# Kernel optimization log

Measured on AMD Instinct MI355X. Metric: run time of the kernel, lower is better.

## Reference

```python
import math
import jax, jax.numpy as jnp
import numpy as np

H = 16
D_MODEL = 1024
D_K = D_MODEL // H


def setup_inputs() -> dict:
    key = jax.random.key(0)
    ks = jax.random.split(key, 12)
    B, S = 4, 2048
    scale = 1.0 / math.sqrt(D_MODEL)
    inp = {
        "query": jax.random.normal(ks[0], (B, S, D_MODEL), jnp.float32),
        "key": jax.random.normal(ks[1], (B, S, D_MODEL), jnp.float32),
        "value": jax.random.normal(ks[2], (B, S, D_MODEL), jnp.float32),
        "mask": jnp.ones((B, 1, 1, S), jnp.int32),
        "Wq": jax.random.normal(ks[3], (D_MODEL, D_MODEL), jnp.float32) * scale,
        "bq": jnp.zeros((D_MODEL,), jnp.float32),
        "Wk": jax.random.normal(ks[4], (D_MODEL, D_MODEL), jnp.float32) * scale,
        "bk": jnp.zeros((D_MODEL,), jnp.float32),
        "Wv": jax.random.normal(ks[5], (D_MODEL, D_MODEL), jnp.float32) * scale,
        "bv": jnp.zeros((D_MODEL,), jnp.float32),
        "Wo": jax.random.normal(ks[6], (D_MODEL, D_MODEL), jnp.float32) * scale,
        "bo": jnp.zeros((D_MODEL,), jnp.float32),
    }
    return inp


def _split_heads(x, W, b):
    # x: (B, S, d_model) -> (B, H, S, d_k); torch Linear: x @ W.T + b
    B, S, _ = x.shape
    y = x @ W.T + b
    return y.reshape(B, S, H, D_K).transpose(0, 2, 1, 3)


def reference(query, key, value, mask, Wq, bq, Wk, bk, Wv, bv, Wo, bo):
    B, Sq, _ = query.shape
    q = _split_heads(query, Wq, bq)   # (B,H,Sq,dk)
    k = _split_heads(key, Wk, bk)     # (B,H,Skv,dk)
    v = _split_heads(value, Wv, bv)   # (B,H,Skv,dk)
    scores = jnp.einsum('bhqd,bhkd->bhqk', q, k) / math.sqrt(D_K)
    scores = jnp.where(mask == 0, jnp.float32(-1e9), scores)
    p_attn = jax.nn.softmax(scores, axis=-1)  # dropout p=0 (eval)
    x = jnp.einsum('bhqk,bhkd->bhqd', p_attn, v)
    x = x.transpose(0, 2, 1, 3).reshape(B, Sq, H * D_K)
    return x @ Wo.T + bo
```

## Files before the change

### kernel.cpp

```cpp
#include <hip/hip_runtime.h>
#include <hip/hip_bf16.h>
#include <stdint.h>

typedef unsigned short u16;
typedef short bf16x8 __attribute__((ext_vector_type(8)));
typedef float f32x4 __attribute__((ext_vector_type(4)));

#define D_MODEL 1024
#define NHEAD 16
#define DK 64
#define SEQ 2048
#define NB 4
#define MTOT (NB * SEQ)

__device__ __forceinline__ u16 f2bf(float f) {
  union { float f; unsigned u; } x; x.f = f;
  unsigned r = x.u + 0x7FFFu + ((x.u >> 16) & 1u);
  return (u16)(r >> 16);
}
#if __has_builtin(__builtin_amdgcn_cvt_pk_bf16_f32)
__device__ __forceinline__ unsigned pkbf(float a, float b) {
  auto r = __builtin_amdgcn_cvt_pk_bf16_f32(a, b);
  union { decltype(r) v; unsigned u; } c; c.v = r; return c.u;
}
#else
__device__ __forceinline__ unsigned pkbf(float a, float b) {
  return (unsigned)f2bf(a) | ((unsigned)f2bf(b) << 16);
}
#endif
#if __has_builtin(__builtin_amdgcn_exp2f)
__device__ __forceinline__ float exp2r(float x) { return __builtin_amdgcn_exp2f(x); }
#else
__device__ __forceinline__ float exp2r(float x) { return exp2f(x); }
#endif
__device__ __forceinline__ void gl_lds16(const u16* g, u16* s) {
  __builtin_amdgcn_global_load_lds(
      (const __attribute__((address_space(1))) void*)g,
      (__attribute__((address_space(3))) void*)s, 16, 0, 0);
}

struct CvtArgs {
  const float4* s[7];
  uint2* d[7];
  int n4[7];
};
__global__ __launch_bounds__(256) void cvt_all(CvtArgs a) {
  const int y = blockIdx.y;
  const float4* s = a.s[y];
  uint2* d = a.d[y];
  const int n4 = a.n4[y];
  for (int i = blockIdx.x * 256 + threadIdx.x; i < n4; i += gridDim.x * 256) {
    float4 x = s[i];
    uint2 o;
    o.x = pkbf(x.x, x.y);
    o.y = pkbf(x.z, x.w);
    d[i] = o;
  }
}
__global__ __launch_bounds__(256) void cvt1(const float4* __restrict__ src,
                                            uint2* __restrict__ dst, int n4) {
  for (int i = blockIdx.x * 256 + threadIdx.x; i < n4; i += gridDim.x * 256) {
    float4 x = src[i];
    uint2 o;
    o.x = pkbf(x.x, x.y);
    o.y = pkbf(x.z, x.w);
    dst[i] = o;
  }
}
__global__ __launch_bounds__(256) void cvt4(const float4* __restrict__ s0,
                                            const float4* __restrict__ s1,
                                            const float4* __restrict__ s2,
                                            const float4* __restrict__ s3,
                                            uint2* __restrict__ dst, int n4each) {
  const float4* s = (blockIdx.y == 0) ? s0 : (blockIdx.y == 1) ? s1
                  : (blockIdx.y == 2) ? s2 : s3;
  uint2* d = dst + (size_t)blockIdx.y * n4each;
  for (int i = blockIdx.x * 256 + threadIdx.x; i < n4each; i += gridDim.x * 256) {
    float4 x = s[i];
    uint2 o;
    o.x = pkbf(x.x, x.y);
    o.y = pkbf(x.z, x.w);
    d[i] = o;
  }
}

template <int MODE>
__device__ __forceinline__ void gemm_body(
    const u16* __restrict__ A, const u16* __restrict__ W,
    const float* __restrict__ bias, void* __restrict__ out, float scale,
    int m0, int n0, u16* smem)
{
  u16* As = smem;
  u16* Bs = smem + 4096;

  const int tid = threadIdx.x;
  const int l = tid & 63, w = tid >> 6;
  const int lq = l & 15, qd = l >> 4;
  const int wm = (w >> 1) << 5, wn = (w & 1) << 6;

  int arow[2], ak8[2], brow[4], bk8[4];
#pragma unroll
  for (int r = 0; r < 2; ++r) {
    int c = r * 256 + tid;
    arow[r] = c >> 3; ak8[r] = (c & 7) ^ (arow[r] & 7);
  }
#pragma unroll
  for (int r = 0; r < 4; ++r) {
    int c = r * 256 + tid;
    brow[r] = c >> 3; bk8[r] = (c & 7) ^ (brow[r] & 7);
  }
  int aoff[2][2], boff[4][2];
#pragma unroll
  for (int i = 0; i < 2; ++i) {
    int mr = wm + (i << 4) + lq;
#pragma unroll
    for (int s = 0; s < 2; ++s)
      aoff[i][s] = (mr << 6) + ((((s << 2) + qd) ^ (mr & 7)) << 3);
  }
#pragma unroll
  for (int j = 0; j < 4; ++j) {
    int nr = wn + (j << 4) + lq;
#pragma unroll
    for (int s = 0; s < 2; ++s)
      boff[j][s] = (nr << 6) + ((((s << 2) + qd) ^ (nr & 7)) << 3);
  }

  const u16* Ab = A + (size_t)m0 * D_MODEL;
  const u16* Bb = W + (size_t)n0 * D_MODEL;

  f32x4 acc[2][4] = {};

  for (int kt = 0; kt < 16; ++kt) {
    const int kbase = kt << 6;
#pragma unroll
    for (int r = 0; r < 2; ++r)
      gl_lds16(Ab + (size_t)arow[r] * D_MODEL + kbase + (ak8[r] << 3), As + ((r * 256 + tid) << 3));
#pragma unroll
    for (int r = 0; r < 4; ++r)
      gl_lds16(Bb + (size_t)brow[r] * D_MODEL + kbase + (bk8[r] << 3), Bs + ((r * 256 + tid) << 3));
    __syncthreads();
#pragma unroll
    for (int s = 0; s < 2; ++s) {
      bf16x8 af[2], bfv[4];
#pragma unroll
      for (int i = 0; i < 2; ++i) af[i] = *(const bf16x8*)(As + aoff[i][s]);
#pragma unroll
      for (int j = 0; j < 4; ++j) bfv[j] = *(const bf16x8*)(Bs + boff[j][s]);
#pragma unroll
      for (int i = 0; i < 2; ++i)
#pragma unroll
        for (int j = 0; j < 4; ++j)
          acc[i][j] = __builtin_amdgcn_mfma_f32_16x16x32_bf16(af[i], bfv[j], acc[i][j], 0, 0, 0);
    }
    __syncthreads();
  }

  if (MODE == 1) {
    u16* Cs = smem;
    u16* outb = (u16*)out;
#pragma unroll
    for (int i = 0; i < 2; ++i)
#pragma unroll
      for (int j = 0; j < 4; ++j) {
        int ml = wm + (i << 4) + (qd << 2);
        int nl = wn + (j << 4) + lq;
        float bj = bias[n0 + nl];
        uint2 pk;
        pk.x = pkbf(acc[i][j][0] + bj, acc[i][j][1] + bj);
        pk.y = pkbf(acc[i][j][2] + bj, acc[i][j][3] + bj);
        *(uint2*)(Cs + nl * 80 + ml) = pk;
      }
    __syncthreads();
    int nl = tid >> 1, sh = (tid & 1) << 5;
    int n = n0 + nl;
    int b_ = m0 >> 11;
    const uint4* src = (const uint4*)(Cs + nl * 80 + sh);
    uint4* dst = (uint4*)(outb +
        (((size_t)b_ * NHEAD + (n >> 6)) * DK + (n & 63)) * SEQ + (m0 & 2047) + sh);
#pragma unroll
    for (int e = 0; e < 4; ++e) dst[e] = src[e];
  } else {
    u16* outb = (u16*)out;
    float* outf = (float*)out;
#pragma unroll
    for (int i = 0; i < 2; ++i)
#pragma unroll
      for (int j = 0; j < 4; ++j) {
        int ml = m0 + wm + (i << 4) + (qd << 2);
        int n = n0 + wn + (j << 4) + lq;
        float bj = bias[n];
#pragma unroll
        for (int r = 0; r < 4; ++r) {
          int m = ml + r;
          float v = (acc[i][j][r] + bj) * scale;
          if (MODE == 0)
            outb[(((size_t)(m >> 11) * NHEAD + (n >> 6)) * SEQ + (m & 2047)) * DK + (n & 63)] = f2bf(v);
          else
            outf[(size_t)m * D_MODEL + n] = v;
        }
      }
  }
}

template <int MODE>
__global__ __launch_bounds__(256, 4) void gemm_bt64(
    const u16* __restrict__ A, const u16* __restrict__ W,
    const float* __restrict__ bias, void* __restrict__ out, float scale)
{
  __shared__ alignas(16) u16 smem[12288];
  gemm_body<MODE>(A, W, bias, out, scale,
                  blockIdx.y << 6, blockIdx.x << 7, smem);
}

__global__ __launch_bounds__(256, 4) void proj_qkv(
    const u16* __restrict__ Cq, const u16* __restrict__ Ck, const u16* __restrict__ Cv,
    const u16* __restrict__ wq, const u16* __restrict__ wk, const u16* __restrict__ wv,
    const float* __restrict__ bq, const float* __restrict__ bk, const float* __restrict__ bv,
    u16* __restrict__ Qb, u16* __restrict__ Kb, u16* __restrict__ Vt, float scq)
{
  __shared__ alignas(16) u16 smem[12288];
  const int z = blockIdx.z;
  const int m0 = blockIdx.y << 6, n0 = blockIdx.x << 7;
  if (z == 0)
    gemm_body<0>(Cq, wq, bq, Qb, scq, m0, n0, smem);
  else if (z == 1)
    gemm_body<0>(Ck, wk, bk, Kb, 1.0f, m0, n0, smem);
  else
    gemm_body<1>(Cv, wv, bv, Vt, 1.0f, m0, n0, smem);
}

__global__ __launch_bounds__(256, 4) void attn_fused(
    const u16* __restrict__ Q,
    const u16* __restrict__ K,
    const u16* __restrict__ Vt,
    const int* __restrict__ mask,
    u16* __restrict__ X)
{
  __shared__ alignas(16) u16 PQ[8192];
  __shared__ alignas(16) u16 Ks[4096];
  __shared__ alignas(16) u16 Vs[5120];
  __shared__ alignas(16) float mbf[64];

  const int tid = threadIdx.x;
  const int l = tid & 63, w = tid >> 6;
  const int lq = l & 15, qd = l >> 4;
  const int bh = blockIdx.y;
  const int q0 = blockIdx.x << 7;
  const int b_ = bh >> 4, h = bh & 15;
  const size_t base = (size_t)bh * SEQ * DK;
  const int wq0 = w << 5;

#pragma unroll
  for (int r = 0; r < 4; ++r) {
    int c = r * 256 + tid;
    int row = c >> 3, k8 = (c & 7) ^ (row & 7);
    gl_lds16(Q + base + (size_t)(q0 + row) * DK + (k8 << 3), PQ + (c << 3));
  }
  {
    unsigned v = (tid < 16) ? 0x3F803F80u : 0u;
    uint2 pk; pk.x = v; pk.y = v;
    *(uint2*)(Vs + 4096 + tid * 4) = pk;
  }
  __syncthreads();

  bf16x8 qf[2][2];
#pragma unroll
  for (int i = 0; i < 2; ++i)
#pragma unroll
    for (int s = 0; s < 2; ++s) {
      int row = wq0 + (i << 4) + lq;
      qf[i][s] = *(const bf16x8*)(PQ + (row << 6) + ((((s << 2) + qd) ^ (row & 7)) << 3));
    }

  f32x4 Ov[2][4] = {};
  f32x4 Ovl[2] = {};

  for (int t = 0; t < 32; ++t) {
    const int kv0 = t << 6;
    __syncthreads();
#pragma unroll
    for (int r = 0; r < 2; ++r) {
      int c = r * 256 + tid;
      int row = c >> 3, k8 = (c & 7) ^ (row & 7);
      gl_lds16(K + base + (size_t)(kv0 + row) * DK + (k8 << 3), Ks + (c << 3));
    }
#pragma unroll
    for (int r = 0; r < 2; ++r) {
      int c = r * 256 + tid;
      int row = c >> 3, k8 = (c & 7) ^ (row & 7);
      gl_lds16(Vt + base + (size_t)row * SEQ + kv0 + (k8 << 3), Vs + (c << 3));
    }
    if (tid < 64)
      mbf[tid] = mask[b_ * SEQ + kv0 + tid] ? 0.0f : -1.44269504e9f;
    __syncthreads();

    float4 m4[4];
#pragma unroll
    for (int jb = 0; jb < 4; ++jb) m4[jb] = *(const float4*)(mbf + (jb << 4) + (qd << 2));

    f32x4 Sc[4][2];
#pragma unroll
    for (int jb = 0; jb < 4; ++jb)
#pragma unroll
      for (int i = 0; i < 2; ++i) {
        Sc[jb][i][0] = m4[jb].x; Sc[jb][i][1] = m4[jb].y;
        Sc[jb][i][2] = m4[jb].z; Sc[jb][i][3] = m4[jb].w;
      }
#pragma unroll
    for (int s = 0; s < 2; ++s) {
      bf16x8 kf[4];
#pragma unroll
      for (int jb = 0; jb < 4; ++jb) {
        int row = (jb << 4) + lq;
        kf[jb] = *(const bf16x8*)(Ks + (row << 6) + ((((s << 2) + qd) ^ (row & 7)) << 3));
      }
#pragma unroll
      for (int jb = 0; jb < 4; ++jb)
#pragma unroll
        for (int i = 0; i < 2; ++i)
          Sc[jb][i] = __builtin_amdgcn_mfma_f32_16x16x32_bf16(kf[jb], qf[i][s], Sc[jb][i], 0, 0, 0);
    }

#pragma unroll
    for (int i = 0; i < 2; ++i) {
      const int prow = wq0 + (i << 4) + lq;
      const int rbase = prow << 6;
      const int rsw = prow & 7;
#pragma unroll
      for (int jb = 0; jb < 4; ++jb) {
        float p0 = exp2r(Sc[jb][i][0]);
        float p1 = exp2r(Sc[jb][i][1]);
        float p2 = exp2r(Sc[jb][i][2]);
        float p3 = exp2r(Sc[jb][i][3]);
        uint2 pk;
        pk.x = pkbf(p0, p1);
        pk.y = pkbf(p2, p3);
        int c = (jb << 1) + (qd >> 1);
        *(uint2*)(PQ + rbase + ((c ^ rsw) << 3) + ((qd & 1) << 2)) = pk;
      }
    }

#pragma unroll
    for (int s = 0; s < 2; ++s) {
      bf16x8 pf[2], vf[4], vf1;
#pragma unroll
      for (int i = 0; i < 2; ++i) {
        int prow = wq0 + (i << 4) + lq;
        pf[i] = *(const bf16x8*)(PQ + (prow << 6) + ((((s << 2) + qd) ^ (prow & 7)) << 3));
      }
#pragma unroll
      for (int j = 0; j < 4; ++j) {
        int row = (j << 4) + lq;
        vf[j] = *(const bf16x8*)(Vs + (row << 6) + ((((s << 2) + qd) ^ (row & 7)) << 3));
      }
      {
        int row = 64 + lq;
        vf1 = *(const bf16x8*)(Vs + (row << 6) + ((((s << 2) + qd) ^ (row & 7)) << 3));
      }
#pragma unroll
      for (int i = 0; i < 2; ++i) {
#pragma unroll
        for (int j = 0; j < 4; ++j)
          Ov[i][j] = __builtin_amdgcn_mfma_f32_16x16x32_bf16(pf[i], vf[j], Ov[i][j], 0, 0, 0);
        Ovl[i] = __builtin_amdgcn_mfma_f32_16x16x32_bf16(pf[i], vf1, Ovl[i], 0, 0, 0);
      }
    }
  }

#pragma unroll
  for (int i = 0; i < 2; ++i) {
    float inv[4];
#pragma unroll
    for (int r = 0; r < 4; ++r) inv[r] = 1.0f / Ovl[i][r];
#pragma unroll
    for (int r = 0; r < 4; ++r) {
      float sc_ = __shfl(inv[r], l & 48);
      int qrow = q0 + wq0 + (i << 4) + (qd << 2) + r;
#pragma unroll
      for (int j = 0; j < 4; ++j)
        X[((size_t)b_ * SEQ + qrow) * D_MODEL + (h << 6) + (j << 4) + lq] =
            f2bf(Ov[i][j][r] * sc_);
    }
  }
}

extern "C" void kernel_launch(void* const* d_in, const int* in_sizes, int n_in,
                              void* d_out, int out_size, void* d_ws, size_t ws_size,
                              hipStream_t stream) {
  const float* query = (const float*)d_in[0];
  const float* key_  = (const float*)d_in[1];
  const float* value = (const float*)d_in[2];
  const int* mask    = (const int*)d_in[3];
  const float* Wq = (const float*)d_in[4];
  const float* bq = (const float*)d_in[5];
  const float* Wk = (const float*)d_in[6];
  const float* bk = (const float*)d_in[7];
  const float* Wv = (const float*)d_in[8];
  const float* bv = (const float*)d_in[9];
  const float* Wo = (const float*)d_in[10];
  const float* bo = (const float*)d_in[11];

  u16* ws16 = (u16*)d_ws;
  const size_t WSZ = (size_t)D_MODEL * D_MODEL;
  const size_t ASZ = (size_t)MTOT * D_MODEL;
  const float SCQ = 0.125f * 1.44269504088896f;

  dim3 blk(256);
  dim3 gg(D_MODEL / 128, MTOT / 64);

  if (ws_size >= (size_t)(4 * WSZ + 4 * ASZ) * 2) {
    u16* wqc = ws16;
    u16* wkc = ws16 + WSZ;
    u16* wvc = ws16 + 2 * WSZ;
    u16* woc = ws16 + 3 * WSZ;
    u16* Cq  = ws16 + 4 * WSZ;
    u16* Ck  = ws16 + 4 * WSZ + ASZ;
    u16* Qb  = ws16 + 4 * WSZ + 2 * ASZ;
    u16* Kb  = ws16 + 4 * WSZ + 3 * ASZ;
    u16* Xb  = Cq;
    u16* Vtb = (u16*)d_out;
    u16* Cv  = (u16*)d_out + ASZ;

    CvtArgs ca;
    ca.s[0] = (const float4*)query; ca.d[0] = (uint2*)Cq;  ca.n4[0] = (int)(ASZ / 4);
    ca.s[1] = (const float4*)key_;  ca.d[1] = (uint2*)Ck;  ca.n4[1] = (int)(ASZ / 4);
    ca.s[2] = (const float4*)value; ca.d[2] = (uint2*)Cv;  ca.n4[2] = (int)(ASZ / 4);
    ca.s[3] = (const float4*)Wq;    ca.d[3] = (uint2*)wqc; ca.n4[3] = (int)(WSZ / 4);
    ca.s[4] = (const float4*)Wk;    ca.d[4] = (uint2*)wkc; ca.n4[4] = (int)(WSZ / 4);
    ca.s[5] = (const float4*)Wv;    ca.d[5] = (uint2*)wvc; ca.n4[5] = (int)(WSZ / 4);
    ca.s[6] = (const float4*)Wo;    ca.d[6] = (uint2*)woc; ca.n4[6] = (int)(WSZ / 4);

    cvt_all<<<dim3(512, 7), blk, 0, stream>>>(ca);
    proj_qkv<<<dim3(D_MODEL / 128, MTOT / 64, 3), blk, 0, stream>>>(
        Cq, Ck, Cv, wqc, wkc, wvc, bq, bk, bv, Qb, Kb, Vtb, SCQ);
    attn_fused<<<dim3(SEQ / 128, NB * NHEAD), blk, 0, stream>>>(Qb, Kb, Vtb, mask, Xb);
    gemm_bt64<2><<<gg, blk, 0, stream>>>(Xb, woc, bo, d_out, 1.0f);
  } else {
    u16* wqc = ws16;
    u16* wkc = ws16 + WSZ;
    u16* wvc = ws16 + 2 * WSZ;
    u16* woc = ws16 + 3 * WSZ;
    u16* C1  = ws16 + 4 * WSZ;
    u16* Qb  = ws16 + 4 * WSZ + ASZ;
    u16* Kb  = ws16 + 4 * WSZ + 2 * ASZ;
    u16* Xb  = C1;
    u16* Vtb = (u16*)d_out;

    cvt4<<<dim3(256, 4), blk, 0, stream>>>((const float4*)Wq, (const float4*)Wk,
                                           (const float4*)Wv, (const float4*)Wo,
                                           (uint2*)wqc, (int)(WSZ / 4));
    cvt1<<<1024, blk, 0, stream>>>((const float4*)query, (uint2*)C1, (int)(ASZ / 4));
    gemm_bt64<0><<<gg, blk, 0, stream>>>(C1, wqc, bq, Qb, SCQ);
    cvt1<<<1024, blk, 0, stream>>>((const float4*)key_, (uint2*)C1, (int)(ASZ / 4));
    gemm_bt64<0><<<gg, blk, 0, stream>>>(C1, wkc, bk, Kb, 1.0f);
    cvt1<<<1024, blk, 0, stream>>>((const float4*)value, (uint2*)C1, (int)(ASZ / 4));
    gemm_bt64<1><<<gg, blk, 0, stream>>>(C1, wvc, bv, Vtb, 1.0f);
    attn_fused<<<dim3(SEQ / 128, NB * NHEAD), blk, 0, stream>>>(Qb, Kb, Vtb, mask, Xb);
    gemm_bt64<2><<<gg, blk, 0, stream>>>(Xb, woc, bo, d_out, 1.0f);
  }
}
```

Measured before the change: 349.6 us.

## Enlarge GEMM tiles to 128x128 and reorder grids for M-major block scheduling

The shared GEMM body moves from a 64x128 to a 128x128 output tile, with each wave computing a 64x64 sub-tile (4x4 MFMA fragments). The aim is more data reuse per LDS load and fewer global loads per FLOP. Grid dimensions for the projection, output GEMM and attention kernels are swapped, so consecutive blocks walk M (or batch-head) first, which changes cache locality of the shared weight and K/V tiles. The cost is a larger shared-memory footprint and more accumulator registers, and the occupancy hint of 4 blocks per CU is dropped. The fallback path reuses cvt_all in place of the removed cvt1/cvt4 kernels.

```diff
diff --git a/kernel.cpp b/kernel.cpp
--- a/kernel.cpp
+++ b/kernel.cpp
@@ -57,32 +57,6 @@
     d[i] = o;
   }
 }
-__global__ __launch_bounds__(256) void cvt1(const float4* __restrict__ src,
-                                            uint2* __restrict__ dst, int n4) {
-  for (int i = blockIdx.x * 256 + threadIdx.x; i < n4; i += gridDim.x * 256) {
-    float4 x = src[i];
-    uint2 o;
-    o.x = pkbf(x.x, x.y);
-    o.y = pkbf(x.z, x.w);
-    dst[i] = o;
-  }
-}
-__global__ __launch_bounds__(256) void cvt4(const float4* __restrict__ s0,
-                                            const float4* __restrict__ s1,
-                                            const float4* __restrict__ s2,
-                                            const float4* __restrict__ s3,
-                                            uint2* __restrict__ dst, int n4each) {
-  const float4* s = (blockIdx.y == 0) ? s0 : (blockIdx.y == 1) ? s1
-                  : (blockIdx.y == 2) ? s2 : s3;
-  uint2* d = dst + (size_t)blockIdx.y * n4each;
-  for (int i = blockIdx.x * 256 + threadIdx.x; i < n4each; i += gridDim.x * 256) {
-    float4 x = s[i];
-    uint2 o;
-    o.x = pkbf(x.x, x.y);
-    o.y = pkbf(x.z, x.w);
-    d[i] = o;
-  }
-}
 
 template <int MODE>
 __device__ __forceinline__ void gemm_body(
@@ -91,63 +65,56 @@
     int m0, int n0, u16* smem)
 {
   u16* As = smem;
-  u16* Bs = smem + 4096;
+  u16* Bs = smem + 8192;
 
   const int tid = threadIdx.x;
   const int l = tid & 63, w = tid >> 6;
-  const int lq = l & 15, qd = l >> 4;
-  const int wm = (w >> 1) << 5, wn = (w & 1) << 6;
-
-  int arow[2], ak8[2], brow[4], bk8[4];
-#pragma unroll
-  for (int r = 0; r < 2; ++r) {
-    int c = r * 256 + tid;
-    arow[r] = c >> 3; ak8[r] = (c & 7) ^ (arow[r] & 7);
-  }
+  const int wm = (w >> 1) << 6, wn = (w & 1) << 6;
+
+  int srow[4], sk8[4], sdst[4];
 #pragma unroll
   for (int r = 0; r < 4; ++r) {
     int c = r * 256 + tid;
-    brow[r] = c >> 3; bk8[r] = (c & 7) ^ (brow[r] & 7);
-  }
-  int aoff[2][2], boff[4][2];
-#pragma unroll
-  for (int i = 0; i < 2; ++i) {
-    int mr = wm + (i << 4) + lq;
-#pragma unroll
-    for (int s = 0; s < 2; ++s)
-      aoff[i][s] = (mr << 6) + ((((s << 2) + qd) ^ (mr & 7)) << 3);
-  }
-#pragma unroll
-  for (int j = 0; j < 4; ++j) {
-    int nr = wn + (j << 4) + lq;
-#pragma unroll
-    for (int s = 0; s < 2; ++s)
-      boff[j][s] = (nr << 6) + ((((s << 2) + qd) ^ (nr & 7)) << 3);
+    srow[r] = c >> 3;
+    sk8[r] = (c & 7) ^ (srow[r] & 7);
+    sdst[r] = c << 3;
+  }
+  int aoff[4][2], boff[4][2];
+#pragma unroll
+  for (int i = 0; i < 4; ++i) {
+    int mr = wm + (i << 4) + (l & 15);
+    int nr = wn + (i << 4) + (l & 15);
+#pragma unroll
+    for (int s = 0; s < 2; ++s) {
+      int kc = (s << 2) + (l >> 4);
+      aoff[i][s] = (mr << 6) + ((kc ^ (mr & 7)) << 3);
+      boff[i][s] = (nr << 6) + ((kc ^ (nr & 7)) << 3);
+    }
   }
 
   const u16* Ab = A + (size_t)m0 * D_MODEL;
   const u16* Bb = W + (size_t)n0 * D_MODEL;
 
-  f32x4 acc[2][4] = {};
+  f32x4 acc[4][4] = {};
 
   for (int kt = 0; kt < 16; ++kt) {
     const int kbase = kt << 6;
 #pragma unroll
-    for (int r = 0; r < 2; ++r)
-      gl_lds16(Ab + (size_t)arow[r] * D_MODEL + kbase + (ak8[r] << 3), As + ((r * 256 + tid) << 3));
-#pragma unroll
     for (int r = 0; r < 4; ++r)
-      gl_lds16(Bb + (size_t)brow[r] * D_MODEL + kbase + (bk8[r] << 3), Bs + ((r * 256 + tid) << 3));
+      gl_lds16(Ab + (size_t)srow[r] * D_MODEL + kbase + (sk8[r] << 3), As + sdst[r]);
+#pragma unroll
+    for (int r = 0; r < 4; ++r)
+      gl_lds16(Bb + (size_t)srow[r] * D_MODEL + kbase + (sk8[r] << 3), Bs + sdst[r]);
     __syncthreads();
 #pragma unroll
     for (int s = 0; s < 2; ++s) {
-      bf16x8 af[2], bfv[4];
-#pragma unroll
-      for (int i = 0; i < 2; ++i) af[i] = *(const bf16x8*)(As + aoff[i][s]);
+      bf16x8 af[4], bfv[4];
+#pragma unroll
+      for (int i = 0; i < 4; ++i) af[i] = *(const bf16x8*)(As + aoff[i][s]);
 #pragma unroll
       for (int j = 0; j < 4; ++j) bfv[j] = *(const bf16x8*)(Bs + boff[j][s]);
 #pragma unroll
-      for (int i = 0; i < 2; ++i)
+      for (int i = 0; i < 4; ++i)
 #pragma unroll
         for (int j = 0; j < 4; ++j)
           acc[i][j] = __builtin_amdgcn_mfma_f32_16x16x32_bf16(af[i], bfv[j], acc[i][j], 0, 0, 0);
@@ -159,35 +126,35 @@
     u16* Cs = smem;
     u16* outb = (u16*)out;
 #pragma unroll
-    for (int i = 0; i < 2; ++i)
+    for (int i = 0; i < 4; ++i)
 #pragma unroll
       for (int j = 0; j < 4; ++j) {
-        int ml = wm + (i << 4) + (qd << 2);
-        int nl = wn + (j << 4) + lq;
+        int sl = wm + (i << 4) + ((l >> 4) << 2);
+        int nl = wn + (j << 4) + (l & 15);
         float bj = bias[n0 + nl];
         uint2 pk;
         pk.x = pkbf(acc[i][j][0] + bj, acc[i][j][1] + bj);
         pk.y = pkbf(acc[i][j][2] + bj, acc[i][j][3] + bj);
-        *(uint2*)(Cs + nl * 80 + ml) = pk;
+        *(uint2*)(Cs + nl * 136 + sl) = pk;
       }
     __syncthreads();
-    int nl = tid >> 1, sh = (tid & 1) << 5;
+    int nl = tid >> 1, sh = (tid & 1) << 6;
     int n = n0 + nl;
     int b_ = m0 >> 11;
-    const uint4* src = (const uint4*)(Cs + nl * 80 + sh);
+    const uint4* src = (const uint4*)(Cs + nl * 136 + sh);
     uint4* dst = (uint4*)(outb +
         (((size_t)b_ * NHEAD + (n >> 6)) * DK + (n & 63)) * SEQ + (m0 & 2047) + sh);
 #pragma unroll
-    for (int e = 0; e < 4; ++e) dst[e] = src[e];
+    for (int e = 0; e < 8; ++e) dst[e] = src[e];
   } else {
     u16* outb = (u16*)out;
     float* outf = (float*)out;
 #pragma unroll
-    for (int i = 0; i < 2; ++i)
+    for (int i = 0; i < 4; ++i)
 #pragma unroll
       for (int j = 0; j < 4; ++j) {
-        int ml = m0 + wm + (i << 4) + (qd << 2);
-        int n = n0 + wn + (j << 4) + lq;
+        int ml = m0 + wm + (i << 4) + ((l >> 4) << 2);
+        int n = n0 + wn + (j << 4) + (l & 15);
         float bj = bias[n];
 #pragma unroll
         for (int r = 0; r < 4; ++r) {
@@ -203,24 +170,24 @@
 }
 
 template <int MODE>
-__global__ __launch_bounds__(256, 4) void gemm_bt64(
+__global__ __launch_bounds__(256) void gemm128(
     const u16* __restrict__ A, const u16* __restrict__ W,
     const float* __restrict__ bias, void* __restrict__ out, float scale)
 {
-  __shared__ alignas(16) u16 smem[12288];
+  __shared__ alignas(16) u16 smem[17408];
   gemm_body<MODE>(A, W, bias, out, scale,
-                  blockIdx.y << 6, blockIdx.x << 7, smem);
-}
-
-__global__ __launch_bounds__(256, 4) void proj_qkv(
+                  blockIdx.x << 7, blockIdx.y << 7, smem);
+}
+
+__global__ __launch_bounds__(256) void proj_qkv(
     const u16* __restrict__ Cq, const u16* __restrict__ Ck, const u16* __restrict__ Cv,
     const u16* __restrict__ wq, const u16* __restrict__ wk, const u16* __restrict__ wv,
     const float* __restrict__ bq, const float* __restrict__ bk, const float* __restrict__ bv,
     u16* __restrict__ Qb, u16* __restrict__ Kb, u16* __restrict__ Vt, float scq)
 {
-  __shared__ alignas(16) u16 smem[12288];
+  __shared__ alignas(16) u16 smem[17408];
   const int z = blockIdx.z;
-  const int m0 = blockIdx.y << 6, n0 = blockIdx.x << 7;
+  const int m0 = blockIdx.x << 7, n0 = blockIdx.y << 7;
   if (z == 0)
     gemm_body<0>(Cq, wq, bq, Qb, scq, m0, n0, smem);
   else if (z == 1)
@@ -244,8 +211,8 @@
   const int tid = threadIdx.x;
   const int l = tid & 63, w = tid >> 6;
   const int lq = l & 15, qd = l >> 4;
-  const int bh = blockIdx.y;
-  const int q0 = blockIdx.x << 7;
+  const int bh = blockIdx.x;
+  const int q0 = blockIdx.y << 7;
   const int b_ = bh >> 4, h = bh & 15;
   const size_t base = (size_t)bh * SEQ * DK;
   const int wq0 = w << 5;
@@ -406,7 +373,7 @@
   const float SCQ = 0.125f * 1.44269504088896f;
 
   dim3 blk(256);
-  dim3 gg(D_MODEL / 128, MTOT / 64);
+  dim3 gg(MTOT / 128, D_MODEL / 128);
 
   if (ws_size >= (size_t)(4 * WSZ + 4 * ASZ) * 2) {
     u16* wqc = ws16;
@@ -431,10 +398,10 @@
     ca.s[6] = (const float4*)Wo;    ca.d[6] = (uint2*)woc; ca.n4[6] = (int)(WSZ / 4);
 
     cvt_all<<<dim3(512, 7), blk, 0, stream>>>(ca);
-    proj_qkv<<<dim3(D_MODEL / 128, MTOT / 64, 3), blk, 0, stream>>>(
+    proj_qkv<<<dim3(MTOT / 128, D_MODEL / 128, 3), blk, 0, stream>>>(
         Cq, Ck, Cv, wqc, wkc, wvc, bq, bk, bv, Qb, Kb, Vtb, SCQ);
-    attn_fused<<<dim3(SEQ / 128, NB * NHEAD), blk, 0, stream>>>(Qb, Kb, Vtb, mask, Xb);
-    gemm_bt64<2><<<gg, blk, 0, stream>>>(Xb, woc, bo, d_out, 1.0f);
+    attn_fused<<<dim3(NB * NHEAD, SEQ / 128), blk, 0, stream>>>(Qb, Kb, Vtb, mask, Xb);
+    gemm128<2><<<gg, blk, 0, stream>>>(Xb, woc, bo, d_out, 1.0f);
   } else {
     u16* wqc = ws16;
     u16* wkc = ws16 + WSZ;
@@ -446,16 +413,25 @@
     u16* Xb  = C1;
     u16* Vtb = (u16*)d_out;
 
-    cvt4<<<dim3(256, 4), blk, 0, stream>>>((const float4*)Wq, (const float4*)Wk,
-                                           (const float4*)Wv, (const float4*)Wo,
-                                           (uint2*)wqc, (int)(WSZ / 4));
-    cvt1<<<1024, blk, 0, stream>>>((const float4*)query, (uint2*)C1, (int)(ASZ / 4));
-    gemm_bt64<0><<<gg, blk, 0, stream>>>(C1, wqc, bq, Qb, SCQ);
-    cvt1<<<1024, blk, 0, stream>>>((const float4*)key_, (uint2*)C1, (int)(ASZ / 4));
-    gemm_bt64<0><<<gg, blk, 0, stream>>>(C1, wkc, bk, Kb, 1.0f);
-    cvt1<<<1024, blk, 0, stream>>>((const float4*)value, (uint2*)C1, (int)(ASZ / 4));
-    gemm_bt64<1><<<gg, blk, 0, stream>>>(C1, wvc, bv, Vtb, 1.0f);
-    attn_fused<<<dim3(SEQ / 128, NB * NHEAD), blk, 0, stream>>>(Qb, Kb, Vtb, mask, Xb);
-    gemm_bt64<2><<<gg, blk, 0, stream>>>(Xb, woc, bo, d_out, 1.0f);
-  }
-}
+    CvtArgs cw;
+    for (int i = 0; i < 7; ++i) { cw.s[i] = (const float4*)Wq; cw.d[i] = (uint2*)wqc; cw.n4[i] = 0; }
+    cw.s[0] = (const float4*)Wq; cw.d[0] = (uint2*)wqc; cw.n4[0] = (int)(WSZ / 4);
+    cw.s[1] = (const float4*)Wk; cw.d[1] = (uint2*)wkc; cw.n4[1] = (int)(WSZ / 4);
+    cw.s[2] = (const float4*)Wv; cw.d[2] = (uint2*)wvc; cw.n4[2] = (int)(WSZ / 4);
+    cw.s[3] = (const float4*)Wo; cw.d[3] = (uint2*)woc; cw.n4[3] = (int)(WSZ / 4);
+
+    cvt_all<<<dim3(512, 4), blk, 0, stream>>>(cw);
+    CvtArgs c1;
+    c1.s[0] = (const float4*)query; c1.d[0] = (uint2*)C1; c1.n4[0] = (int)(ASZ / 4);
+    cvt_all<<<dim3(1024, 1), blk, 0, stream>>>(c1);
+    gemm128<0><<<gg, blk, 0, stream>>>(C1, wqc, bq, Qb, SCQ);
+    c1.s[0] = (const float4*)key_;
+    cvt_all<<<dim3(1024, 1), blk, 0, stream>>>(c1);
+    gemm128<0><<<gg, blk, 0, stream>>>(C1, wkc, bk, Kb, 1.0f);
+    c1.s[0] = (const float4*)value;
+    cvt_all<<<dim3(1024, 1), blk, 0, stream>>>(c1);
+    gemm128<1><<<gg, blk, 0, stream>>>(C1, wvc, bv, Vtb, 1.0f);
+    attn_fused<<<dim3(NB * NHEAD, SEQ / 128), blk, 0, stream>>>(Qb, Kb, Vtb, mask, Xb);
+    gemm128<2><<<gg, blk, 0, stream>>>(Xb, woc, bo, d_out, 1.0f);
+  }
+}
```

Result: no change. 349.2 us (-0.1%).
